# Kernel tuning notes

Hardware: AMD Instinct MI355X
Metric: run time of the kernel (lower is better)

## Reference

```python
import jax, jax.numpy as jnp
import numpy as np

G = 16          # horizontal stripes
K = 4           # latents per stripe
TEMP = 0.125
TOPK_RATIO = 0.125
GATE_THR = 0.05
EPS = 1e-6
KSZ = 3


def setup_inputs() -> dict:
    key = jax.random.key(0)
    k1, k2 = jax.random.split(key)
    x = jax.random.normal(k1, (64, 256, 64, 44), dtype=jnp.float32)
    latent_basis = jax.random.normal(k2, (G, K, 256), dtype=jnp.float32)
    return {"x": x, "latent_basis": latent_basis}


def _avg_pool3(x):
    # x: [n, g, c, sh, w]; 3x3 avg pool, stride 1, pad 1, count_include_pad=True
    s = jax.lax.reduce_window(x, 0.0, jax.lax.add,
                              (1, 1, 1, KSZ, KSZ), (1, 1, 1, 1, 1),
                              [(0, 0), (0, 0), (0, 0), (1, 1), (1, 1)])
    return s / float(KSZ * KSZ)


def _l2norm(v, axis=-1):
    return v / jnp.maximum(jnp.linalg.norm(v, axis=axis, keepdims=True), 1e-12)


def reference(x, latent_basis):
    n, c, h, w = x.shape
    sh = h // G
    p = sh * w
    # split into horizontal stripes: [n, g, c, sh, w]
    xr = x.reshape(n, c, G, sh, w).transpose(0, 2, 1, 3, 4)
    support_feat = _avg_pool3(xr)
    feat_flat = xr.transpose(0, 1, 3, 4, 2).reshape(n, G, p, c)          # ngpc
    support_flat = support_feat.transpose(0, 1, 3, 4, 2).reshape(n, G, p, c)

    # active mask from detached feature energy
    e = jax.lax.stop_gradient(xr).astype(jnp.float32)
    fe = jnp.mean(e * e, axis=2)                                          # n g sh w
    fe = fe / jnp.maximum(jnp.max(fe, axis=(-2, -1), keepdims=True), EPS)
    active = (fe > GATE_THR).astype(jnp.float32)
    fallback = (fe > 0).astype(jnp.float32)
    use_fb = jnp.sum(active, axis=(-2, -1), keepdims=True) <= 0
    active = jnp.where(use_fb, fallback, active).reshape(n, G, p)

    # cosine-similarity routing
    sfn = _l2norm(support_flat)
    lbn = _l2norm(latent_basis)                                           # g k c
    logits = jnp.einsum('ngpc,gkc->ngpk', sfn, lbn) / TEMP
    route_prob = jax.nn.softmax(logits, axis=-1)
    support = route_prob * active[..., None]                              # n g p k
    pool_w = support / jnp.maximum(jnp.sum(support, axis=2, keepdims=True), EPS)
    tokens = jnp.einsum('ngpk,ngpc->ngkc', pool_w, feat_flat)
    tokens = tokens.transpose(0, 3, 1, 2).reshape(n, c, G * K)            # n c (g k)

    # top-k presence
    kk = max(1, min(p, int(p * TOPK_RATIO)))
    topv, _ = jax.lax.top_k(support.transpose(0, 1, 3, 2), kk)            # n g k kk
    presence = jnp.mean(topv, axis=-1).reshape(n, G * K)
    presence = presence / jnp.maximum(jnp.sum(presence, axis=1, keepdims=True), EPS)

    # scatter per-stripe maps back into full-resolution zero tensors
    eye = jnp.eye(G, dtype=support.dtype)
    loc_s = support.reshape(n, G, sh, w, K).transpose(0, 1, 4, 2, 3)      # n g k sh w
    loc_p = pool_w.reshape(n, G, sh, w, K).transpose(0, 1, 4, 2, 3)
    smap = jnp.einsum('ngksw,gG->ngkGsw', loc_s, eye).reshape(n, G * K, h, w)
    pmap = jnp.einsum('ngksw,gG->ngkGsw', loc_p, eye).reshape(n, G * K, h, w)
    support_flat_global = smap.transpose(0, 2, 3, 1).reshape(n, h * w, G * K)
    pool_weights_flat_global = pmap.transpose(0, 2, 3, 1).reshape(n, h * w, G * K)

    return (tokens.astype(x.dtype), presence.astype(x.dtype),
            support_flat_global.astype(x.dtype), pool_weights_flat_global.astype(x.dtype))
```

## Files before the change

### kernel.cpp

```cpp
#include <hip/hip_runtime.h>
#include <math.h>

#define GG   16
#define KK   4
#define NN   64
#define CC   256
#define SHH  4
#define WW   44
#define PP   176
#define HWSZ 2816
#define CHW  720896
#define TOPKK 22

template<int CTRL, int RMASK>
__device__ __forceinline__ float dpp0(float v) {
    return __int_as_float(__builtin_amdgcn_update_dpp(
        0, __float_as_int(v), CTRL, RMASK, 0xF, true));
}
__device__ __forceinline__ float nbrL(float v) { return dpp0<0x138, 0xF>(v); }
__device__ __forceinline__ float nbrR(float v) { return dpp0<0x130, 0xF>(v); }

__device__ __forceinline__ float wave_sum63(float v) {
    v += dpp0<0x111, 0xF>(v);
    v += dpp0<0x112, 0xF>(v);
    v += dpp0<0x114, 0xF>(v);
    v += dpp0<0x118, 0xF>(v);
    v += dpp0<0x142, 0xA>(v);
    v += dpp0<0x143, 0xC>(v);
    return v;
}
__device__ __forceinline__ float bcast63(float v) {
    return __int_as_float(__builtin_amdgcn_readlane(__float_as_int(v), 63));
}
__device__ __forceinline__ float wave_sum_all(float v) { return bcast63(wave_sum63(v)); }

__device__ __forceinline__ float wave_max_nn(float v) {
    v = fmaxf(v, dpp0<0x111, 0xF>(v));
    v = fmaxf(v, dpp0<0x112, 0xF>(v));
    v = fmaxf(v, dpp0<0x114, 0xF>(v));
    v = fmaxf(v, dpp0<0x118, 0xF>(v));
    v = fmaxf(v, dpp0<0x142, 0xA>(v));
    v = fmaxf(v, dpp0<0x143, 0xC>(v));
    return bcast63(v);
}

__global__ __launch_bounds__(512, 8) void routing_kernel(
    const float* __restrict__ x, const float* __restrict__ lb_raw,
    float* __restrict__ pres_ws,
    float4* __restrict__ outS, float4* __restrict__ outP,
    float* __restrict__ tok_out) {
    const int g = blockIdx.x;
    const int n = blockIdx.y;
    const int tid = threadIdx.x;
    const int w = __builtin_amdgcn_readfirstlane(tid >> 6);
    const int lane = tid & 63;
    const bool al = lane < WW;

    __shared__ float4 pd[8][PP];
    __shared__ float2 pnf[8][PP];
    __shared__ float4 lbn_lds[CC];
    __shared__ float redA[4], redB[4], zred[4][4];
    float4* sup4 = pd[2];
    float4* pw4  = pd[4];

    if (w < 4) {
        const float* row = lb_raw + ((size_t)g * KK + w) * CC;
        float v0 = row[lane], v1 = row[lane + 64], v2 = row[lane + 128], v3 = row[lane + 192];
        float ss = v0 * v0 + v1 * v1 + v2 * v2 + v3 * v3;
        float tot = wave_sum_all(ss);
        float sc = (1.0f / 9.0f) / fmaxf(sqrtf(tot), 1e-12f);
        float* dst = (float*)lbn_lds;
        dst[lane * 4 + w]         = v0 * sc;
        dst[(lane + 64) * 4 + w]  = v1 * sc;
        dst[(lane + 128) * 4 + w] = v2 * sc;
        dst[(lane + 192) * 4 + w] = v3 * sc;
    }
    __syncthreads();

    const float* xb = x + (size_t)n * CHW + g * PP;
    const int c0 = w * 32;

    float4 dk[4];
    float nr[4] = {0, 0, 0, 0}, fe[4] = {0, 0, 0, 0};
    #pragma unroll
    for (int s = 0; s < 4; ++s) dk[s] = make_float4(0, 0, 0, 0);

    const float* xp = xb + (size_t)c0 * HWSZ + lane;
    float c0r = 0, c1r = 0, c2r = 0, c3r = 0;
    float n0r = 0, n1r = 0, n2r = 0, n3r = 0;
    if (al) {
        c0r = xp[0]; c1r = xp[44]; c2r = xp[88]; c3r = xp[132];
        n0r = xp[HWSZ]; n1r = xp[HWSZ + 44]; n2r = xp[HWSZ + 88]; n3r = xp[HWSZ + 132];
    }
    xp += 2 * HWSZ;
    #pragma unroll 1
    for (int i = 0; i < 32; ++i) {
        float f0 = 0, f1 = 0, f2 = 0, f3 = 0;
        if (i < 30 && al) { f0 = xp[0]; f1 = xp[44]; f2 = xp[88]; f3 = xp[132]; }
        xp += HWSZ;
        float4 lbv = lbn_lds[c0 + i];
        fe[0] += c0r * c0r; fe[1] += c1r * c1r; fe[2] += c2r * c2r; fe[3] += c3r * c3r;
        float h0 = c0r + nbrL(c0r) + nbrR(c0r);
        float h1 = c1r + nbrL(c1r) + nbrR(c1r);
        float h2 = c2r + nbrL(c2r) + nbrR(c2r);
        float h3 = c3r + nbrL(c3r) + nbrR(c3r);
        float p0 = h0 + h1;
        float p1 = p0 + h2;
        float t23 = h2 + h3;
        float p2 = h1 + t23;
        float p3 = t23;
        nr[0] += p0 * p0; nr[1] += p1 * p1; nr[2] += p2 * p2; nr[3] += p3 * p3;
        dk[0].x += p0 * lbv.x; dk[0].y += p0 * lbv.y; dk[0].z += p0 * lbv.z; dk[0].w += p0 * lbv.w;
        dk[1].x += p1 * lbv.x; dk[1].y += p1 * lbv.y; dk[1].z += p1 * lbv.z; dk[1].w += p1 * lbv.w;
        dk[2].x += p2 * lbv.x; dk[2].y += p2 * lbv.y; dk[2].z += p2 * lbv.z; dk[2].w += p2 * lbv.w;
        dk[3].x += p3 * lbv.x; dk[3].y += p3 * lbv.y; dk[3].z += p3 * lbv.z; dk[3].w += p3 * lbv.w;
        c0r = n0r; c1r = n1r; c2r = n2r; c3r = n3r;
        n0r = f0; n1r = f1; n2r = f2; n3r = f3;
    }
    if (al) {
        #pragma unroll
        for (int s = 0; s < 4; ++s) {
            pd[w][s * 44 + lane]  = dk[s];
            pnf[w][s * 44 + lane] = make_float2(nr[s], fe[s]);
        }
    }
    __syncthreads();

    if (tid < PP) {
        float4 a = pd[0][tid];
        #pragma unroll
        for (int ww = 1; ww < 8; ++ww) {
            float4 b = pd[ww][tid];
            a.x += b.x; a.y += b.y; a.z += b.z; a.w += b.w;
        }
        pd[0][tid] = a;
    } else if (tid >= 256 && tid < 256 + PP) {
        const int p = tid - 256;
        float2 a = pnf[0][p];
        #pragma unroll
        for (int ww = 1; ww < 8; ++ww) {
            float2 b = pnf[ww][p];
            a.x += b.x; a.y += b.y;
        }
        pnf[0][p] = a;
    }
    __syncthreads();

    const int s4 = w & 3;
    const int pix = s4 * 44 + (al ? lane : 0);
    float4 dv = pd[0][pix];
    float2 nf = pnf[0][pix];
    float nrm = nf.x;
    float fev = nf.y * (1.0f / 256.0f);

    float fmw = wave_max_nn(al ? fev : 0.0f);
    if (w < 4 && lane == 0) redA[s4] = fmw;
    __syncthreads();
    float femax = fmaxf(fmaxf(redA[0], redA[1]), fmaxf(redA[2], redA[3]));
    float den = fmaxf(femax, 1e-6f);
    bool pa = al && ((fev / den) > 0.05f);
    unsigned long long bl = __ballot((int)pa);
    if (w < 4 && lane == 0) redB[s4] = (float)__popcll(bl);
    __syncthreads();
    float cnt = redB[0] + redB[1] + redB[2] + redB[3];
    float actv = pa ? 1.0f : 0.0f;
    if (cnt <= 0.0f) actv = (al && (fev > 0.0f)) ? 1.0f : 0.0f;

    float inv = 72.0f / fmaxf(sqrtf(nrm), 9e-12f);
    float L0 = dv.x * inv, L1 = dv.y * inv, L2 = dv.z * inv, L3 = dv.w * inv;
    float mx = fmaxf(fmaxf(L0, L1), fmaxf(L2, L3));
    float e0 = expf(L0 - mx), e1 = expf(L1 - mx), e2 = expf(L2 - mx), e3 = expf(L3 - mx);
    float esum = e0 + e1 + e2 + e3;
    float sc = actv / esum;
    float s0 = e0 * sc, s1 = e1 * sc, s2 = e2 * sc, s3 = e3 * sc;

    float z0 = wave_sum63(s0), z1 = wave_sum63(s1), z2 = wave_sum63(s2), z3 = wave_sum63(s3);
    if (w < 4 && lane == 63) { zred[s4][0] = z0; zred[s4][1] = z1; zred[s4][2] = z2; zred[s4][3] = z3; }
    __syncthreads();
    float Z0 = zred[0][0] + zred[1][0] + zred[2][0] + zred[3][0];
    float Z1 = zred[0][1] + zred[1][1] + zred[2][1] + zred[3][1];
    float Z2 = zred[0][2] + zred[1][2] + zred[2][2] + zred[3][2];
    float Z3 = zred[0][3] + zred[1][3] + zred[2][3] + zred[3][3];
    float q0 = s0 / fmaxf(Z0, 1e-6f);
    float q1 = s1 / fmaxf(Z1, 1e-6f);
    float q2 = s2 / fmaxf(Z2, 1e-6f);
    float q3 = s3 / fmaxf(Z3, 1e-6f);

    if (w < 4 && al) {
        sup4[pix] = make_float4(s0, s1, s2, s3);
        pw4[pix]  = make_float4(q0, q1, q2, q3);
    }
    __syncthreads();

    if (w < 4) {
        const float* supf = (const float*)sup4;
        const int k = w;
        float v0 = supf[lane * 4 + k];
        float v1 = supf[(lane + 64) * 4 + k];
        float v2 = (lane < PP - 128) ? supf[(lane + 128) * 4 + k] : -1e30f;
        float tks = 0.0f;
        for (int it = 0; it < TOPKK; ++it) {
            float lm = fmaxf(v0, fmaxf(v1, v2));
            float M = wave_max_nn(lm);
            tks += M;
            unsigned long long mk = __ballot((int)(lm == M));
            int src = __ffsll(mk) - 1;
            if (lane == src) {
                if (v0 == M)      v0 = -1e30f;
                else if (v1 == M) v1 = -1e30f;
                else              v2 = -1e30f;
            }
        }
        if (lane == 0) pres_ws[(size_t)n * 64 + g * KK + k] = tks * (1.0f / (float)TOPKK);
    }

    {
        const size_t obase = ((size_t)n * HWSZ + (size_t)g * PP) * 16;
        const float4 z = make_float4(0, 0, 0, 0);
        #pragma unroll 1
        for (int j = tid; j < PP * 16; j += 512) {
            const int px = j >> 4, q = j & 15;
            const bool hit = (q == g);
            outS[obase + j] = hit ? sup4[px] : z;
            outP[obase + j] = hit ? pw4[px]  : z;
        }
    }

    {
        float4 pwa = pw4[lane];
        float4 pwb = pw4[lane + 64];
        float4 pwc = (lane < 48) ? pw4[lane + 128] : make_float4(0, 0, 0, 0);
        const float* xq = xb + (size_t)c0 * HWSZ + lane;
        float* tokg = tok_out + ((size_t)n * CC + c0) * 64 + g * KK;

        float a0 = xq[0];
        float a1 = xq[64];
        float a2 = (lane < 48) ? xq[128] : 0.0f;
        xq += HWSZ;
        #pragma unroll 1
        for (int i = 0; i < 32; ++i) {
            float b0 = 0, b1 = 0, b2 = 0;
            if (i < 31) {
                b0 = xq[0]; b1 = xq[64];
                if (lane < 48) b2 = xq[128];
            }
            xq += HWSZ;
            float t0 = a0 * pwa.x + a1 * pwb.x + a2 * pwc.x;
            float t1 = a0 * pwa.y + a1 * pwb.y + a2 * pwc.y;
            float t2 = a0 * pwa.z + a1 * pwb.z + a2 * pwc.z;
            float t3 = a0 * pwa.w + a1 * pwb.w + a2 * pwc.w;
            t0 = wave_sum63(t0); t1 = wave_sum63(t1); t2 = wave_sum63(t2); t3 = wave_sum63(t3);
            if (lane == 63) {
                *(float4*)(tokg + (size_t)i * 64) = make_float4(t0, t1, t2, t3);
            }
            a0 = b0; a1 = b1; a2 = b2;
        }
    }
}

__global__ __launch_bounds__(64) void presence_kernel(
    const float* __restrict__ pres_ws, float* __restrict__ outp) {
    const int n = blockIdx.x;
    const int lane = threadIdx.x;
    float v = pres_ws[(size_t)n * 64 + lane];
    float tot = wave_sum_all(v);
    outp[(size_t)n * 64 + lane] = v / fmaxf(tot, 1e-6f);
}

extern "C" void kernel_launch(void* const* d_in, const int* in_sizes, int n_in,
                              void* d_out, int out_size, void* d_ws, size_t ws_size,
                              hipStream_t stream) {
    const float* x = (const float*)d_in[0];
    const float* lb = (const float*)d_in[1];
    float* ws = (float*)d_ws;
    float* pres_ws = ws;

    float* out = (float*)d_out;
    float* tok  = out;
    float* pres = out + 1048576;
    float* outS = out + 1052672;
    float* outP = outS + 11534336;

    routing_kernel<<<dim3(GG, NN), 512, 0, stream>>>(
        x, lb, pres_ws, (float4*)outS, (float4*)outP, tok);
    presence_kernel<<<NN, 64, 0, stream>>>(pres_ws, pres);
}
```

Before: 337.2 us.

## Vectorize token x loads as float4 with deeper prefetch and split zero-fill to upper waves

Result: no change. 335.0 us (-0.7%).

```diff
diff --git a/kernel.cpp b/kernel.cpp
--- a/kernel.cpp
+++ b/kernel.cpp
@@ -62,6 +62,7 @@
     __shared__ float redA[4], redB[4], zred[4][4];
     float4* sup4 = pd[2];
     float4* pw4  = pd[4];
+    float4* pwT  = pd[6];
 
     if (w < 4) {
         const float* row = lb_raw + ((size_t)g * KK + w) * CC;
@@ -187,8 +188,10 @@
     float q3 = s3 / fmaxf(Z3, 1e-6f);
 
     if (w < 4 && al) {
+        float4 qv = make_float4(q0, q1, q2, q3);
         sup4[pix] = make_float4(s0, s1, s2, s3);
-        pw4[pix]  = make_float4(q0, q1, q2, q3);
+        pw4[pix]  = qv;
+        pwT[(pix & 3) * 44 + (pix >> 2)] = qv;
     }
     __syncthreads();
 
@@ -212,13 +215,13 @@
             }
         }
         if (lane == 0) pres_ws[(size_t)n * 64 + g * KK + k] = tks * (1.0f / (float)TOPKK);
-    }
-
-    {
+    } else {
         const size_t obase = ((size_t)n * HWSZ + (size_t)g * PP) * 16;
         const float4 z = make_float4(0, 0, 0, 0);
+        const int t0i = tid - 256;
         #pragma unroll 1
-        for (int j = tid; j < PP * 16; j += 512) {
+        for (int m = 0; m < 11; ++m) {
+            const int j = t0i + m * 256;
             const int px = j >> 4, q = j & 15;
             const bool hit = (q == g);
             outS[obase + j] = hit ? sup4[px] : z;
@@ -227,33 +230,34 @@
     }
 
     {
-        float4 pwa = pw4[lane];
-        float4 pwb = pw4[lane + 64];
-        float4 pwc = (lane < 48) ? pw4[lane + 128] : make_float4(0, 0, 0, 0);
-        const float* xq = xb + (size_t)c0 * HWSZ + lane;
+        const bool a4 = lane < 44;
+        float4 pwa = make_float4(0, 0, 0, 0), pwb = pwa, pwc = pwa, pwd = pwa;
+        if (a4) {
+            pwa = pwT[lane];
+            pwb = pwT[44 + lane];
+            pwc = pwT[88 + lane];
+            pwd = pwT[132 + lane];
+        }
+        const float4* xq4 = (const float4*)(xb + (size_t)c0 * HWSZ) + lane;
+        float4 tA = make_float4(0, 0, 0, 0), tB = tA, tC = tA;
+        if (a4) { tA = xq4[0]; tB = xq4[704]; tC = xq4[1408]; }
+        xq4 += 3 * 704;
         float* tokg = tok_out + ((size_t)n * CC + c0) * 64 + g * KK;
 
-        float a0 = xq[0];
-        float a1 = xq[64];
-        float a2 = (lane < 48) ? xq[128] : 0.0f;
-        xq += HWSZ;
         #pragma unroll 1
         for (int i = 0; i < 32; ++i) {
-            float b0 = 0, b1 = 0, b2 = 0;
-            if (i < 31) {
-                b0 = xq[0]; b1 = xq[64];
-                if (lane < 48) b2 = xq[128];
-            }
-            xq += HWSZ;
-            float t0 = a0 * pwa.x + a1 * pwb.x + a2 * pwc.x;
-            float t1 = a0 * pwa.y + a1 * pwb.y + a2 * pwc.y;
-            float t2 = a0 * pwa.z + a1 * pwb.z + a2 * pwc.z;
-            float t3 = a0 * pwa.w + a1 * pwb.w + a2 * pwc.w;
+            float4 tF = make_float4(0, 0, 0, 0);
+            if (i < 29 && a4) tF = xq4[0];
+            xq4 += 704;
+            float t0 = tA.x * pwa.x + tA.y * pwb.x + tA.z * pwc.x + tA.w * pwd.x;
+            float t1 = tA.x * pwa.y + tA.y * pwb.y + tA.z * pwc.y + tA.w * pwd.y;
+            float t2 = tA.x * pwa.z + tA.y * pwb.z + tA.z * pwc.z + tA.w * pwd.z;
+            float t3 = tA.x * pwa.w + tA.y * pwb.w + tA.z * pwc.w + tA.w * pwd.w;
             t0 = wave_sum63(t0); t1 = wave_sum63(t1); t2 = wave_sum63(t2); t3 = wave_sum63(t3);
             if (lane == 63) {
                 *(float4*)(tokg + (size_t)i * 64) = make_float4(t0, t1, t2, t3);
             }
-            a0 = b0; a1 = b1; a2 = b2;
+            tA = tB; tB = tC; tC = tF;
         }
     }
 }
```
